# Performance work log

Hardware: AMD Instinct MI355X
Metric: run time of the kernel (lower is better)

Reference implementation:

```python
import jax, jax.numpy as jnp
import numpy as np

B, C, H, W = 4, 512, 64, 64
C8 = C // 8


def setup_inputs() -> dict:
    key = jax.random.key(0)
    ks = jax.random.split(key, 8)
    return {
        "x": jax.random.normal(ks[0], (B, C, H, W), jnp.float32),
        "wb": jax.random.normal(ks[1], (C8, C), jnp.float32) * 0.05,
        "bb": jax.random.normal(ks[2], (C8,), jnp.float32) * 0.05,
        "wc": jax.random.normal(ks[3], (C8, C), jnp.float32) * 0.05,
        "bc": jax.random.normal(ks[4], (C8,), jnp.float32) * 0.05,
        "wd": jax.random.normal(ks[5], (C, C), jnp.float32) * 0.05,
        "bd": jax.random.normal(ks[6], (C,), jnp.float32) * 0.05,
        "alpha": jax.random.normal(ks[7], (1,), jnp.float32),
    }


def reference(x, wb, bb, wc, bc, wd, bd, alpha):
    b, c, h, w = x.shape
    n = h * w
    xf = x.reshape(b, c, n)  # [B, C, N]
    # 1x1 convs == per-pixel channel matmuls
    feat_b = jnp.einsum('kc,bcn->bkn', wb, xf) + bb[:, None]  # [B, C/8, N]
    feat_c = jnp.einsum('kc,bcn->bkn', wc, xf) + bc[:, None]  # [B, C/8, N]
    # attention_s[n, m] = softmax_m( feat_b[:, n] . feat_c[:, m] )  (no scaling, as in source)
    scores = jnp.einsum('bkn,bkm->bnm', feat_b, feat_c)  # [B, N, N]
    attn = jax.nn.softmax(scores, axis=-1)
    feat_d = jnp.einsum('oc,bcn->bon', wd, xf) + bd[:, None]  # [B, C, N]
    # feat_e = bmm(feat_d, attn^T): fe[c, n] = sum_m fd[c, m] * attn[n, m]
    feat_e = jnp.einsum('bcm,bnm->bcn', feat_d, attn).reshape(b, c, h, w)
    return alpha[0] * feat_e + x
```

## Files before the change

kernel.cpp:

```cpp
#include <hip/hip_runtime.h>
#include <hip/hip_bf16.h>

#define NB 4
#define CC 512
#define CK 64
#define NN 4096

typedef unsigned short u16;
typedef __attribute__((ext_vector_type(8))) __bf16 bf16x8;
typedef __attribute__((ext_vector_type(4))) float f32x4;
typedef __attribute__((ext_vector_type(4))) unsigned int u32x4;
typedef __attribute__((ext_vector_type(8))) unsigned short u16x8;
typedef __attribute__((ext_vector_type(4))) unsigned short u16x4;

__device__ __forceinline__ u16 f2b(float f) {
  union { float f; unsigned u; } x; x.f = f;
  unsigned r = x.u + 0x7fffu + ((x.u >> 16) & 1u);
  return (u16)(r >> 16);
}
__device__ __forceinline__ float b2f(u16 u) {
  union { unsigned u; float f; } x; x.u = ((unsigned)u) << 16; return x.f;
}
__device__ __forceinline__ u16 cvt_bf16(float f) {
  union { __bf16 h; u16 u; } c; c.h = (__bf16)f; return c.u;
}
__device__ __forceinline__ float fast_exp2(float x) {
  float r;
  asm("v_exp_f32 %0, %1" : "=v"(r) : "v"(x));
  return r;
}
__device__ __forceinline__ void lds_barrier() {
  asm volatile("s_waitcnt lgkmcnt(0)" ::: "memory");
  __builtin_amdgcn_s_barrier();
}

#define MFMA16(a, b, c) __builtin_amdgcn_mfma_f32_16x16x32_bf16((a), (b), (c), 0, 0, 0)

__global__ __launch_bounds__(256) void proj_qk(
    const float* __restrict__ x,
    const float* __restrict__ wb, const float* __restrict__ bb,
    const float* __restrict__ wc, const float* __restrict__ bc,
    u16* __restrict__ Qhi, u16* __restrict__ Qlo,
    u16* __restrict__ Khi, u16* __restrict__ Klo)
{
  const int tid = threadIdx.x;
  const int n0 = blockIdx.x * 64;
  const int which = blockIdx.y;
  const int b = blockIdx.z;
  const float* w   = which ? wc : wb;
  const float* bia = which ? bc : bb;
  u16* oh = which ? Khi : Qhi;
  u16* ol = which ? Klo : Qlo;
  const float qsc = which ? 1.0f : 1.44269504088896340736f;

  __shared__ u16 Wh[64][40], Wl[64][40], Xh[64][40], Xl[64][40];

  const int lane = tid & 63, wid = tid >> 6;
  const int wr = wid >> 1, wn = wid & 1;
  const int l15 = lane & 15, lk = (lane >> 4) * 8;

  f32x4 acc[2][2] = {};

  for (int kk = 0; kk < CC; kk += 32) {
    {
      const int row = tid >> 2, c0 = (tid & 3) * 8;
      const float* src = w + (size_t)row * CC + kk + c0;
#pragma unroll
      for (int i = 0; i < 8; ++i) {
        float v = src[i];
        u16 h = f2b(v);
        Wh[row][c0 + i] = h;
        Wl[row][c0 + i] = f2b(v - b2f(h));
      }
    }
    {
      const int cc2 = tid >> 3, j0 = (tid & 7) * 8;
      const float* src = x + ((size_t)b * CC + kk + cc2) * NN + n0 + j0;
#pragma unroll
      for (int i = 0; i < 8; ++i) {
        float v = src[i];
        u16 h = f2b(v);
        Xh[j0 + i][cc2] = h;
        Xl[j0 + i][cc2] = f2b(v - b2f(h));
      }
    }
    __syncthreads();
#pragma unroll
    for (int fi = 0; fi < 2; ++fi) {
      const int ar = wr * 32 + fi * 16 + l15;
      bf16x8 ah = *(const bf16x8*)&Wh[ar][lk];
      bf16x8 al = *(const bf16x8*)&Wl[ar][lk];
#pragma unroll
      for (int fj = 0; fj < 2; ++fj) {
        const int br = wn * 32 + fj * 16 + l15;
        bf16x8 bh = *(const bf16x8*)&Xh[br][lk];
        bf16x8 bl = *(const bf16x8*)&Xl[br][lk];
        acc[fi][fj] = MFMA16(ah, bh, acc[fi][fj]);
        acc[fi][fj] = MFMA16(ah, bl, acc[fi][fj]);
        acc[fi][fj] = MFMA16(al, bh, acc[fi][fj]);
      }
    }
    __syncthreads();
  }

#pragma unroll
  for (int fi = 0; fi < 2; ++fi) {
    const int d0 = wr * 32 + fi * 16 + (lane >> 4) * 4;
#pragma unroll
    for (int fj = 0; fj < 2; ++fj) {
      const int n = n0 + wn * 32 + fj * 16 + l15;
      u16x4 vh, vl;
#pragma unroll
      for (int r = 0; r < 4; ++r) {
        float v = (acc[fi][fj][r] + bia[d0 + r]) * qsc;
        u16 h = f2b(v);
        vh[r] = h;
        vl[r] = f2b(v - b2f(h));
      }
      *(u16x4*)&oh[((size_t)b * NN + n) * CK + d0] = vh;
      *(u16x4*)&ol[((size_t)b * NN + n) * CK + d0] = vl;
    }
  }
}

__global__ __launch_bounds__(256) void proj_v(
    const float* __restrict__ x,
    const float* __restrict__ wd, const float* __restrict__ bd,
    u16* __restrict__ Vt)
{
  const int tid = threadIdx.x;
  const int n0 = blockIdx.x * 64;
  const int o0 = blockIdx.y * 64;
  const int b = blockIdx.z;

  __shared__ u16 Wt[64][40], Xt[64][40];
  const int lane = tid & 63, wid = tid >> 6;
  const int wr = wid >> 1, wn = wid & 1;
  const int l15 = lane & 15, lk = (lane >> 4) * 8;

  f32x4 acc[2][2] = {};
  for (int kk = 0; kk < CC; kk += 32) {
    {
      const int row = tid >> 2, c0 = (tid & 3) * 8;
      const float* src = wd + (size_t)(o0 + row) * CC + kk + c0;
#pragma unroll
      for (int i = 0; i < 8; ++i) Wt[row][c0 + i] = f2b(src[i]);
    }
    {
      const int cc2 = tid >> 3, j0 = (tid & 7) * 8;
      const float* src = x + ((size_t)b * CC + kk + cc2) * NN + n0 + j0;
#pragma unroll
      for (int i = 0; i < 8; ++i) Xt[j0 + i][cc2] = f2b(src[i]);
    }
    __syncthreads();
#pragma unroll
    for (int fi = 0; fi < 2; ++fi) {
      bf16x8 a = *(const bf16x8*)&Wt[wr * 32 + fi * 16 + l15][lk];
#pragma unroll
      for (int fj = 0; fj < 2; ++fj) {
        bf16x8 bv = *(const bf16x8*)&Xt[wn * 32 + fj * 16 + l15][lk];
        acc[fi][fj] = MFMA16(a, bv, acc[fi][fj]);
      }
    }
    __syncthreads();
  }
#pragma unroll
  for (int fi = 0; fi < 2; ++fi) {
    const int d0 = o0 + wr * 32 + fi * 16 + (lane >> 4) * 4;
#pragma unroll
    for (int fj = 0; fj < 2; ++fj) {
      const int n = n0 + wn * 32 + fj * 16 + l15;
#pragma unroll
      for (int r = 0; r < 4; ++r)
        Vt[((size_t)b * CC + d0 + r) * NN + n] = f2b(acc[fi][fj][r] + bd[d0 + r]);
    }
  }
}

struct alignas(16) AttnLds {
  u16 kh[64][64];
  u16 kl[64][64];
  float s[64][68];
  u16 p[64][64];
  float m[64];
  float l[64];
  float sc[64];
};

__global__ __launch_bounds__(256, 2) void attn(
    const u16* __restrict__ Qhi, const u16* __restrict__ Qlo,
    const u16* __restrict__ Khi, const u16* __restrict__ Klo,
    const u16* __restrict__ Vt,
    const float* __restrict__ x, const float* __restrict__ alpha,
    float* __restrict__ out)
{
  __shared__ AttnLds L;
  const int tid = threadIdx.x;
  const int lane = tid & 63, wid = tid >> 6;
  const int bid = blockIdx.x;
  const int b = (bid >> 1) & 3;
  const int qt = bid >> 3;
  const int ohalf = bid & 1;
  const int q0 = qt * 64;
  const int l15 = lane & 15;
  const int lk8 = (lane >> 4) * 8;

  const int srow = tid >> 2;
  const int sch  = (tid & 3) * 16;
  const int ssw0 = sch ^ ((srow & 7) << 3);
  const int ssw1 = (sch + 8) ^ ((srow & 7) << 3);

  bf16x8 qah[2], qal[2];
  {
    const size_t qg = ((size_t)b * NN + q0 + wid * 16 + l15) * CK + lk8;
    qah[0] = *(const bf16x8*)&Qhi[qg];
    qah[1] = *(const bf16x8*)&Qhi[qg + 32];
    qal[0] = *(const bf16x8*)&Qlo[qg];
    qal[1] = *(const bf16x8*)&Qlo[qg + 32];
  }
  {
    const size_t g = ((size_t)b * NN + srow) * CK + sch;
    *(u32x4*)&L.kh[srow][ssw0] = *(const u32x4*)&Khi[g];
    *(u32x4*)&L.kh[srow][ssw1] = *(const u32x4*)&Khi[g + 8];
    *(u32x4*)&L.kl[srow][ssw0] = *(const u32x4*)&Klo[g];
    *(u32x4*)&L.kl[srow][ssw1] = *(const u32x4*)&Klo[g + 8];
  }
  if (tid < 64) { L.m[tid] = -__builtin_huge_valf(); L.l[tid] = 0.f; }

  const u16* vbase = Vt + ((size_t)b * CC + ohalf * 256 + wid * 64 + l15) * NN + lk8;

  f32x4 accO[4][4] = {};

  __syncthreads();

  for (int t = 0; t < 64; ++t) {
    const int m0 = t * 64;
    const bool hasNext = (t < 63);

    u32x4 kh0, kh1, kl0, kl1;
    if (hasNext) {
      const size_t g = ((size_t)b * NN + m0 + 64 + srow) * CK + sch;
      kh0 = *(const u32x4*)&Khi[g];
      kh1 = *(const u32x4*)&Khi[g + 8];
      kl0 = *(const u32x4*)&Klo[g];
      kl1 = *(const u32x4*)&Klo[g + 8];
    }
    bf16x8 vr[2][4];
#pragma unroll
    for (int f_ = 0; f_ < 4; ++f_)
#pragma unroll
      for (int ks = 0; ks < 2; ++ks)
        vr[ks][f_] = *(const bf16x8*)(vbase + (size_t)f_ * 16 * NN + m0 + ks * 32);

    __builtin_amdgcn_s_setprio(1);
#pragma unroll
    for (int fj = 0; fj < 4; ++fj) {
      f32x4 s = {};
#pragma unroll
      for (int ks = 0; ks < 2; ++ks) {
        const int k = ks * 32 + lk8;
        const int br = fj * 16 + l15;
        bf16x8 bh = *(const bf16x8*)&L.kh[br][k ^ ((br & 7) << 3)];
        bf16x8 bl = *(const bf16x8*)&L.kl[br][k ^ ((br & 7) << 3)];
        s = MFMA16(qah[ks], bh, s);
        s = MFMA16(qah[ks], bl, s);
        s = MFMA16(qal[ks], bh, s);
      }
      const int r0 = wid * 16 + (lane >> 4) * 4, c0 = fj * 16 + l15;
#pragma unroll
      for (int r = 0; r < 4; ++r) L.s[r0 + r][c0] = s[r];
    }
    __builtin_amdgcn_s_setprio(0);
    lds_barrier();

    if (hasNext) {
      *(u32x4*)&L.kh[srow][ssw0] = kh0;
      *(u32x4*)&L.kh[srow][ssw1] = kh1;
      *(u32x4*)&L.kl[srow][ssw0] = kl0;
      *(u32x4*)&L.kl[srow][ssw1] = kl1;
    }
    {
      const int row = srow, sub = tid & 3;
      const float* sr = &L.s[row][sch];
      f32x4 a0 = *(const f32x4*)&sr[0];
      f32x4 a1 = *(const f32x4*)&sr[4];
      f32x4 a2 = *(const f32x4*)&sr[8];
      f32x4 a3 = *(const f32x4*)&sr[12];
      float mx = fmaxf(fmaxf(fmaxf(a0[0], a0[1]), fmaxf(a0[2], a0[3])),
                       fmaxf(fmaxf(a1[0], a1[1]), fmaxf(a1[2], a1[3])));
      mx = fmaxf(mx, fmaxf(fmaxf(fmaxf(a2[0], a2[1]), fmaxf(a2[2], a2[3])),
                           fmaxf(fmaxf(a3[0], a3[1]), fmaxf(a3[2], a3[3]))));
      mx = fmaxf(mx, __shfl_xor(mx, 1));
      mx = fmaxf(mx, __shfl_xor(mx, 2));
      const float mOld = L.m[row];
      const bool grow = (mx > mOld + 11.5f);
      const float mNew = grow ? mx : mOld;
      float pv[16];
      float sum = 0.f;
#pragma unroll
      for (int j = 0; j < 4; ++j) { pv[j]      = fast_exp2(a0[j] - mNew); sum += pv[j]; }
#pragma unroll
      for (int j = 0; j < 4; ++j) { pv[4 + j]  = fast_exp2(a1[j] - mNew); sum += pv[4 + j]; }
#pragma unroll
      for (int j = 0; j < 4; ++j) { pv[8 + j]  = fast_exp2(a2[j] - mNew); sum += pv[8 + j]; }
#pragma unroll
      for (int j = 0; j < 4; ++j) { pv[12 + j] = fast_exp2(a3[j] - mNew); sum += pv[12 + j]; }
      sum += __shfl_xor(sum, 1);
      sum += __shfl_xor(sum, 2);
      const float scf = grow ? fast_exp2(mOld - mNew) : 1.0f;
      if (sub == 0) {
        if (grow) L.m[row] = mNew;
        L.l[row] = L.l[row] * scf + sum;
        L.sc[row] = scf;
      }
      u16x8 pb0, pb1;
#pragma unroll
      for (int j = 0; j < 8; ++j) pb0[j] = cvt_bf16(pv[j]);
#pragma unroll
      for (int j = 0; j < 8; ++j) pb1[j] = cvt_bf16(pv[8 + j]);
      *(u16x8*)&L.p[row][ssw0] = pb0;
      *(u16x8*)&L.p[row][ssw1] = pb1;
    }
    lds_barrier();

    {
      f32x4 scv[4];
      bool need = false;
#pragma unroll
      for (int f_ = 0; f_ < 4; ++f_) {
        scv[f_] = *(const f32x4*)&L.sc[f_ * 16 + (lane >> 4) * 4];
        need |= (scv[f_][0] != 1.0f) | (scv[f_][1] != 1.0f) |
                (scv[f_][2] != 1.0f) | (scv[f_][3] != 1.0f);
      }
      if (__any(need)) {
#pragma unroll
        for (int f_ = 0; f_ < 4; ++f_)
#pragma unroll
          for (int fj = 0; fj < 4; ++fj)
#pragma unroll
            for (int r = 0; r < 4; ++r)
              accO[f_][fj][r] *= scv[f_][r];
      }
    }
    __builtin_amdgcn_s_setprio(1);
#pragma unroll
    for (int ks = 0; ks < 2; ++ks) {
      const int k = ks * 32 + lk8;
      bf16x8 a[4];
#pragma unroll
      for (int f_ = 0; f_ < 4; ++f_) {
        const int ar = f_ * 16 + l15;
        a[f_] = *(const bf16x8*)&L.p[ar][k ^ ((ar & 7) << 3)];
      }
#pragma unroll
      for (int fj = 0; fj < 4; ++fj)
#pragma unroll
        for (int f_ = 0; f_ < 4; ++f_)
          accO[f_][fj] = MFMA16(a[f_], vr[ks][fj], accO[f_][fj]);
    }
    __builtin_amdgcn_s_setprio(0);
  }
  __syncthreads();
  const float al = alpha[0];
#pragma unroll
  for (int f_ = 0; f_ < 4; ++f_) {
    const int r0 = f_ * 16 + (lane >> 4) * 4;
    const float rl0 = 1.f / L.l[r0],     rl1 = 1.f / L.l[r0 + 1];
    const float rl2 = 1.f / L.l[r0 + 2], rl3 = 1.f / L.l[r0 + 3];
    const int n_ = q0 + r0;
#pragma unroll
    for (int fj = 0; fj < 4; ++fj) {
      const int c_ = ohalf * 256 + wid * 64 + fj * 16 + l15;
      const size_t g = ((size_t)b * CC + c_) * NN + n_;
      f32x4 xv = *(const f32x4*)&x[g];
      f32x4 ov;
      ov[0] = fmaf(al, accO[f_][fj][0] * rl0, xv[0]);
      ov[1] = fmaf(al, accO[f_][fj][1] * rl1, xv[1]);
      ov[2] = fmaf(al, accO[f_][fj][2] * rl2, xv[2]);
      ov[3] = fmaf(al, accO[f_][fj][3] * rl3, xv[3]);
      *(f32x4*)&out[g] = ov;
    }
  }
}

extern "C" void kernel_launch(void* const* d_in, const int* in_sizes, int n_in,
                              void* d_out, int out_size, void* d_ws, size_t ws_size,
                              hipStream_t stream) {
  const float* x     = (const float*)d_in[0];
  const float* wb    = (const float*)d_in[1];
  const float* bb    = (const float*)d_in[2];
  const float* wc    = (const float*)d_in[3];
  const float* bc    = (const float*)d_in[4];
  const float* wd    = (const float*)d_in[5];
  const float* bd    = (const float*)d_in[6];
  const float* alpha = (const float*)d_in[7];
  float* out = (float*)d_out;

  u16* Qhi = (u16*)d_ws;
  u16* Qlo = Qhi + (size_t)NB * NN * CK;
  u16* Khi = Qlo + (size_t)NB * NN * CK;
  u16* Klo = Khi + (size_t)NB * NN * CK;
  u16* Vt  = Klo + (size_t)NB * NN * CK;

  proj_qk<<<dim3(NN / 64, 2, NB), 256, 0, stream>>>(x, wb, bb, wc, bc, Qhi, Qlo, Khi, Klo);
  proj_v<<<dim3(NN / 64, CC / 64, NB), 256, 0, stream>>>(x, wd, bd, Vt);
  attn<<<dim3(512), 256, 0, stream>>>(Qhi, Qlo, Khi, Klo, Vt, x, alpha, out);
}
```

Before: 231.5 us.

## Fuse Q and K projections into one kernel, use hardware bf16 convert

The Q/K projection kernel now computes both the wb and wc projections in a single block, so each x tile is loaded and split into hi/lo bf16 once instead of twice, and the grid shrinks accordingly. Manual round-to-nearest bf16 conversion is replaced with the native bf16 cast throughout. The attention kernel's launch bounds drop the minimum-blocks hint, giving the compiler more register freedom at possible occupancy cost. The fused kernel uses more LDS and registers per block and has half as many blocks.

```diff
diff --git a/kernel.cpp b/kernel.cpp
--- a/kernel.cpp
+++ b/kernel.cpp
@@ -13,11 +13,6 @@
 typedef __attribute__((ext_vector_type(8))) unsigned short u16x8;
 typedef __attribute__((ext_vector_type(4))) unsigned short u16x4;
 
-__device__ __forceinline__ u16 f2b(float f) {
-  union { float f; unsigned u; } x; x.f = f;
-  unsigned r = x.u + 0x7fffu + ((x.u >> 16) & 1u);
-  return (u16)(r >> 16);
-}
 __device__ __forceinline__ float b2f(u16 u) {
   union { unsigned u; float f; } x; x.u = ((unsigned)u) << 16; return x.f;
 }
@@ -45,32 +40,37 @@
 {
   const int tid = threadIdx.x;
   const int n0 = blockIdx.x * 64;
-  const int which = blockIdx.y;
-  const int b = blockIdx.z;
-  const float* w   = which ? wc : wb;
-  const float* bia = which ? bc : bb;
-  u16* oh = which ? Khi : Qhi;
-  u16* ol = which ? Klo : Qlo;
-  const float qsc = which ? 1.0f : 1.44269504088896340736f;
-
-  __shared__ u16 Wh[64][40], Wl[64][40], Xh[64][40], Xl[64][40];
+  const int b = blockIdx.y;
+
+  __shared__ u16 Wbh[64][40], Wbl[64][40], Wch[64][40], Wcl[64][40];
+  __shared__ u16 Xh[64][40], Xl[64][40];
 
   const int lane = tid & 63, wid = tid >> 6;
   const int wr = wid >> 1, wn = wid & 1;
   const int l15 = lane & 15, lk = (lane >> 4) * 8;
 
-  f32x4 acc[2][2] = {};
+  f32x4 accb[2][2] = {}, accc[2][2] = {};
 
   for (int kk = 0; kk < CC; kk += 32) {
-    {
-      const int row = tid >> 2, c0 = (tid & 3) * 8;
-      const float* src = w + (size_t)row * CC + kk + c0;
+    const int row = tid >> 2, c0 = (tid & 3) * 8;
+    {
+      const float* src = wb + (size_t)row * CC + kk + c0;
 #pragma unroll
       for (int i = 0; i < 8; ++i) {
         float v = src[i];
-        u16 h = f2b(v);
-        Wh[row][c0 + i] = h;
-        Wl[row][c0 + i] = f2b(v - b2f(h));
+        u16 h = cvt_bf16(v);
+        Wbh[row][c0 + i] = h;
+        Wbl[row][c0 + i] = cvt_bf16(v - b2f(h));
+      }
+    }
+    {
+      const float* src = wc + (size_t)row * CC + kk + c0;
+#pragma unroll
+      for (int i = 0; i < 8; ++i) {
+        float v = src[i];
+        u16 h = cvt_bf16(v);
+        Wch[row][c0 + i] = h;
+        Wcl[row][c0 + i] = cvt_bf16(v - b2f(h));
       }
     }
     {
@@ -79,30 +79,36 @@
 #pragma unroll
       for (int i = 0; i < 8; ++i) {
         float v = src[i];
-        u16 h = f2b(v);
+        u16 h = cvt_bf16(v);
         Xh[j0 + i][cc2] = h;
-        Xl[j0 + i][cc2] = f2b(v - b2f(h));
+        Xl[j0 + i][cc2] = cvt_bf16(v - b2f(h));
       }
     }
     __syncthreads();
 #pragma unroll
     for (int fi = 0; fi < 2; ++fi) {
       const int ar = wr * 32 + fi * 16 + l15;
-      bf16x8 ah = *(const bf16x8*)&Wh[ar][lk];
-      bf16x8 al = *(const bf16x8*)&Wl[ar][lk];
+      bf16x8 abh = *(const bf16x8*)&Wbh[ar][lk];
+      bf16x8 abl = *(const bf16x8*)&Wbl[ar][lk];
+      bf16x8 ach = *(const bf16x8*)&Wch[ar][lk];
+      bf16x8 acl = *(const bf16x8*)&Wcl[ar][lk];
 #pragma unroll
       for (int fj = 0; fj < 2; ++fj) {
         const int br = wn * 32 + fj * 16 + l15;
         bf16x8 bh = *(const bf16x8*)&Xh[br][lk];
         bf16x8 bl = *(const bf16x8*)&Xl[br][lk];
-        acc[fi][fj] = MFMA16(ah, bh, acc[fi][fj]);
-        acc[fi][fj] = MFMA16(ah, bl, acc[fi][fj]);
-        acc[fi][fj] = MFMA16(al, bh, acc[fi][fj]);
+        accb[fi][fj] = MFMA16(abh, bh, accb[fi][fj]);
+        accb[fi][fj] = MFMA16(abh, bl, accb[fi][fj]);
+        accb[fi][fj] = MFMA16(abl, bh, accb[fi][fj]);
+        accc[fi][fj] = MFMA16(ach, bh, accc[fi][fj]);
+        accc[fi][fj] = MFMA16(ach, bl, accc[fi][fj]);
+        accc[fi][fj] = MFMA16(acl, bh, accc[fi][fj]);
       }
     }
     __syncthreads();
   }
 
+  const float qsc = 1.44269504088896340736f;
 #pragma unroll
   for (int fi = 0; fi < 2; ++fi) {
     const int d0 = wr * 32 + fi * 16 + (lane >> 4) * 4;
@@ -112,13 +118,22 @@
       u16x4 vh, vl;
 #pragma unroll
       for (int r = 0; r < 4; ++r) {
-        float v = (acc[fi][fj][r] + bia[d0 + r]) * qsc;
-        u16 h = f2b(v);
+        float v = (accb[fi][fj][r] + bb[d0 + r]) * qsc;
+        u16 h = cvt_bf16(v);
         vh[r] = h;
-        vl[r] = f2b(v - b2f(h));
-      }
-      *(u16x4*)&oh[((size_t)b * NN + n) * CK + d0] = vh;
-      *(u16x4*)&ol[((size_t)b * NN + n) * CK + d0] = vl;
+        vl[r] = cvt_bf16(v - b2f(h));
+      }
+      *(u16x4*)&Qhi[((size_t)b * NN + n) * CK + d0] = vh;
+      *(u16x4*)&Qlo[((size_t)b * NN + n) * CK + d0] = vl;
+#pragma unroll
+      for (int r = 0; r < 4; ++r) {
+        float v = accc[fi][fj][r] + bc[d0 + r];
+        u16 h = cvt_bf16(v);
+        vh[r] = h;
+        vl[r] = cvt_bf16(v - b2f(h));
+      }
+      *(u16x4*)&Khi[((size_t)b * NN + n) * CK + d0] = vh;
+      *(u16x4*)&Klo[((size_t)b * NN + n) * CK + d0] = vl;
     }
   }
 }
@@ -144,13 +159,13 @@
       const int row = tid >> 2, c0 = (tid & 3) * 8;
       const float* src = wd + (size_t)(o0 + row) * CC + kk + c0;
 #pragma unroll
-      for (int i = 0; i < 8; ++i) Wt[row][c0 + i] = f2b(src[i]);
+      for (int i = 0; i < 8; ++i) Wt[row][c0 + i] = cvt_bf16(src[i]);
     }
     {
       const int cc2 = tid >> 3, j0 = (tid & 7) * 8;
       const float* src = x + ((size_t)b * CC + kk + cc2) * NN + n0 + j0;
 #pragma unroll
-      for (int i = 0; i < 8; ++i) Xt[j0 + i][cc2] = f2b(src[i]);
+      for (int i = 0; i < 8; ++i) Xt[j0 + i][cc2] = cvt_bf16(src[i]);
     }
     __syncthreads();
 #pragma unroll
@@ -172,7 +187,7 @@
       const int n = n0 + wn * 32 + fj * 16 + l15;
 #pragma unroll
       for (int r = 0; r < 4; ++r)
-        Vt[((size_t)b * CC + d0 + r) * NN + n] = f2b(acc[fi][fj][r] + bd[d0 + r]);
+        Vt[((size_t)b * CC + d0 + r) * NN + n] = cvt_bf16(acc[fi][fj][r] + bd[d0 + r]);
     }
   }
 }
@@ -187,7 +202,7 @@
   float sc[64];
 };
 
-__global__ __launch_bounds__(256, 2) void attn(
+__global__ __launch_bounds__(256) void attn(
     const u16* __restrict__ Qhi, const u16* __restrict__ Qlo,
     const u16* __restrict__ Khi, const u16* __restrict__ Klo,
     const u16* __restrict__ Vt,
@@ -402,7 +417,7 @@
   u16* Klo = Khi + (size_t)NB * NN * CK;
   u16* Vt  = Klo + (size_t)NB * NN * CK;
 
-  proj_qk<<<dim3(NN / 64, 2, NB), 256, 0, stream>>>(x, wb, bb, wc, bc, Qhi, Qlo, Khi, Klo);
+  proj_qk<<<dim3(NN / 64, NB), 256, 0, stream>>>(x, wb, bb, wc, bc, Qhi, Qlo, Khi, Klo);
   proj_v<<<dim3(NN / 64, CC / 64, NB), 256, 0, stream>>>(x, wd, bd, Vt);
   attn<<<dim3(512), 256, 0, stream>>>(Qhi, Qlo, Khi, Klo, Vt, x, alpha, out);
 }
```

Result: slower. 370.2 us (+59.9%).
